# Kernel optimization log

Measured on AMD Instinct MI355X. Metric: run time of the kernel, lower is better.

The kernel has to match this reference:

```python
import jax, jax.numpy as jnp
import numpy as np

GRAPH_NUM = 2
HOP_K = 2
NODE_EMB_DIM = 16
INPUT_DIM = 2
HIDDEN = 64
B, N = 8, 400
IN_FEAT = INPUT_DIM + HIDDEN                      # 66, input to each MetaDGCN
I_DIM = (GRAPH_NUM * HOP_K + 1) * IN_FEAT         # 330


def setup_inputs() -> dict:
    key = jax.random.key(0)
    ks = jax.random.split(key, 8)
    x = jax.random.normal(ks[0], (B, N, INPUT_DIM), dtype=jnp.float32)
    state = jax.random.normal(ks[1], (B, N, HIDDEN), dtype=jnp.float32)
    graphs = jax.random.uniform(ks[2], (GRAPH_NUM, B, N, N), dtype=jnp.float32)
    # row-normalize like asym_adj so message passing is stable
    graphs = graphs / graphs.sum(-1, keepdims=True)
    node_emb = jax.random.normal(ks[3], (B, N, NODE_EMB_DIM), dtype=jnp.float32)
    s = 1.0 / np.sqrt(I_DIM)
    Wg = jax.random.normal(ks[4], (NODE_EMB_DIM, I_DIM, 2 * HIDDEN), dtype=jnp.float32) * s
    bg = jax.random.normal(ks[5], (NODE_EMB_DIM, 2 * HIDDEN), dtype=jnp.float32) * 0.1
    Wc = jax.random.normal(ks[6], (NODE_EMB_DIM, I_DIM, HIDDEN), dtype=jnp.float32) * s
    bc = jax.random.normal(ks[7], (NODE_EMB_DIM, HIDDEN), dtype=jnp.float32) * 0.1
    return {"x": x, "state": state, "graphs": graphs, "node_emb": node_emb,
            "Wg": Wg, "bg": bg, "Wc": Wc, "bc": bc}


def meta_dgcn(x, graphs, node_emb, weights_pool, bias_pool):
    # multi-hop propagation over each dynamic graph (GCN: 'bnm,bmd->bnd')
    out = [x]
    for i in range(GRAPH_NUM):
        x1 = x
        for _ in range(HOP_K):
            x1 = jnp.einsum('bnm,bmd->bnd', graphs[i], x1)
            out.append(x1)
    h = jnp.concatenate(out, axis=-1)                          # [B,N,I_DIM]
    # meta-generated per-node weights and bias
    weights = jnp.einsum('bnd,dio->bnio', node_emb, weights_pool)  # [B,N,I,O]
    bias = jnp.einsum('bnd,do->bno', node_emb, bias_pool)
    return jnp.einsum('bni,bnio->bno', h, weights) + bias


def reference(x, state, graphs, node_emb, Wg, bg, Wc, bc):
    # GRU-style meta-graph recurrent cell (MetaDGCRU)
    xs = jnp.concatenate([x, state], axis=-1)                  # [B,N,IN_FEAT]
    zr = jax.nn.sigmoid(meta_dgcn(xs, graphs, node_emb, Wg, bg))
    z, r = jnp.split(zr, 2, axis=-1)
    xrs = jnp.concatenate([x, r * state], axis=-1)
    hc = jnp.tanh(meta_dgcn(xrs, graphs, node_emb, Wc, bc))
    h = z * state + (1.0 - z) * hc                             # [B,N,HIDDEN]
    return h
```

## Files before the change

kernel.cpp:

```cpp
#include <hip/hip_runtime.h>
#include <hip/hip_bf16.h>
#include <math.h>

#define Bb 8
#define Nn 400
#define GN 2
#define INF 66
#define IDIM 330
#define KP 352
#define HID 64
#define EMB 16
#define NKP 416
#define XTR 80
constexpr int M = Bb * Nn;

typedef __attribute__((ext_vector_type(8))) short short8;
typedef __attribute__((ext_vector_type(4))) float f32x4;

__device__ __forceinline__ ushort f2bf(float f) {
    union { float f; unsigned u; } v; v.f = f;
    unsigned u = v.u;
    unsigned r = (u + 0x7FFFu + ((u >> 16) & 1u)) >> 16;
    return (ushort)r;
}

#define GBLKS 10400
__global__ void k_prep(const float* __restrict__ G, const float* __restrict__ Wg,
                       const float* __restrict__ Wc, const float* __restrict__ x,
                       const float* __restrict__ state,
                       ushort* __restrict__ Gbf, ushort* __restrict__ WgT,
                       ushort* __restrict__ WcT, ushort* __restrict__ Hbf,
                       ushort* __restrict__ XTin) {
    __shared__ float Tw[32][65];
    __shared__ ushort Tc[64][XTR + 1];
    int bid = blockIdx.x;
    if (bid < GBLKS) {
        size_t idx = (size_t)bid * 256 + threadIdx.x;
        int k = (int)(idx % NKP);
        size_t row = idx / NKP;
        Gbf[idx] = (k < Nn) ? f2bf(G[row * Nn + k]) : (ushort)0;
        return;
    }
    bid -= GBLKS;
    if (bid < 352 + 176) {
        const float* W; ushort* WT; int O;
        if (bid < 352) { W = Wg; WT = WgT; O = 128; }
        else           { bid -= 352; W = Wc; WT = WcT; O = 64; }
        const int k0 = (bid % 11) * 32;
        const int c0 = (bid / 11) * 64;
        const int d = c0 / O, o0 = c0 % O;
        for (int e = threadIdx.x; e < 2048; e += 256) {
            int kk = e >> 6, oo = e & 63;
            int k = k0 + kk;
            Tw[kk][oo] = (k < IDIM) ? W[((size_t)d * IDIM + k) * O + o0 + oo] : 0.f;
        }
        __syncthreads();
        for (int e = threadIdx.x; e < 2048; e += 256) {
            int cc = e >> 5, kk = e & 31;
            WT[(size_t)(c0 + cc) * KP + k0 + kk] = f2bf(Tw[kk][cc]);
        }
        return;
    }
    bid -= 528;
    const int b = bid / 7;
    const int k0 = (bid % 7) * 64;
    for (int e = threadIdx.x; e < 64 * XTR; e += 256) {
        int kk = e / XTR, c = e % XTR;
        int k = k0 + kk;
        ushort bf = 0;
        if (k < Nn && c < INF) {
            float v = (c < 2) ? x[((size_t)b * Nn + k) * 2 + c]
                              : state[((size_t)b * Nn + k) * HID + c - 2];
            bf = f2bf(v);
            Hbf[((size_t)b * Nn + k) * KP + c] = bf;
        }
        Tc[kk][c] = bf;
    }
    for (int e = threadIdx.x; e < 64 * 22; e += 256) {
        int kk = e / 22, c = 330 + e % 22;
        int k = k0 + kk;
        if (k < Nn) Hbf[((size_t)b * Nn + k) * KP + c] = 0;
    }
    __syncthreads();
    for (int e = threadIdx.x; e < XTR * 64; e += 256) {
        int c = e / 64, kk = e % 64;
        int k = k0 + kk;
        if (k < NKP) XTin[((size_t)b * XTR + c) * NKP + k] = Tc[kk][c];
    }
}

__global__ __launch_bounds__(64) void k_hop(const ushort* __restrict__ Gbf,
                      const ushort* __restrict__ XT,
                      ushort* __restrict__ Hbf, ushort* __restrict__ XTnext,
                      int out_base, int xt_per_g) {
    const int b = blockIdx.y, g = blockIdx.z;
    const int row0 = blockIdx.x * 16;
    const int lane = threadIdx.x;
    const int lr = lane & 15, kq = lane >> 4;

    const ushort* Gb = Gbf + (size_t)(g * Bb + b) * Nn * NKP;
    const ushort* Xb = XT + (size_t)((xt_per_g ? g * Bb : 0) + b) * XTR * NKP;
    const ushort* Grow = Gb + (size_t)(row0 + lr) * NKP;

    f32x4 acc[5] = {};
#pragma unroll
    for (int ks = 0; ks < 13; ++ks) {
        short8 af = *(const short8*)(Grow + ks * 32 + kq * 8);
#pragma unroll
        for (int n = 0; n < 5; ++n) {
            short8 bv = *(const short8*)(Xb + (size_t)(n * 16 + lr) * NKP + ks * 32 + kq * 8);
            acc[n] = __builtin_amdgcn_mfma_f32_16x16x32_bf16(af, bv, acc[n], 0, 0, 0);
        }
    }

    const int rbase = row0 + kq * 4;
    ushort* Hout = Hbf + (size_t)b * Nn * KP + out_base + g * 132;
#pragma unroll
    for (int n = 0; n < 5; ++n) {
        int col = n * 16 + lr;
        if (col < INF) {
#pragma unroll
            for (int r = 0; r < 4; ++r)
                Hout[(size_t)(rbase + r) * KP + col] = f2bf(acc[n][r]);
        }
    }
    if (XTnext) {
        ushort* Xn = XTnext + (size_t)(g * Bb + b) * XTR * NKP;
#pragma unroll
        for (int n = 0; n < 5; ++n) {
            int col = n * 16 + lr;
            ushort4 w;
#pragma unroll
            for (int r = 0; r < 4; ++r)
                w[r] = (col < INF) ? f2bf(acc[n][r]) : (ushort)0;
            *(ushort4*)(Xn + (size_t)col * NKP + rbase) = w;
        }
    }
}

template <int O>
__global__ __launch_bounds__(256, 3) void k_meta_fused(const ushort* __restrict__ Hbf,
        const ushort* __restrict__ WT, const float* __restrict__ emb,
        float* __restrict__ P) {
    constexpr int NB = O / 32;
    constexpr int PB = O / 64;
    __shared__ ushort As[2][64][40];
    __shared__ ushort Bs[2][2][O][40];
    const int ds = blockIdx.x;
    const int bm = blockIdx.y * 64;
    const int t = threadIdx.x;
    const int wid = t >> 6, lane = t & 63;
    const int wm = wid >> 1, wn = wid & 1;
    const int lr = lane & 15, kq = lane >> 4;

    const int ar = t >> 2, akc = (t & 3) * 8;
    const ushort* srcA = Hbf + (size_t)(bm + ar) * KP + akc;
    const ushort* srcB[2][PB];
    int brow[PB], bkc[PB];
#pragma unroll
    for (int p = 0; p < PB; ++p) {
        int chunk = t + p * 256;
        brow[p] = chunk >> 2; bkc[p] = (chunk & 3) * 8;
#pragma unroll
        for (int j = 0; j < 2; ++j)
            srcB[j][p] = WT + ((size_t)(ds * 2 + j) * O + brow[p]) * KP + bkc[p];
    }

    short8 ra, rb[2][PB];
    ra = *(const short8*)srcA;
#pragma unroll
    for (int j = 0; j < 2; ++j)
#pragma unroll
        for (int p = 0; p < PB; ++p) rb[j][p] = *(const short8*)srcB[j][p];

    f32x4 seg[2][2][NB] = {};

    for (int ks = 0; ks < 11; ++ks) {
        const int buf = ks & 1;
        *(short8*)&As[buf][ar][akc] = ra;
#pragma unroll
        for (int j = 0; j < 2; ++j)
#pragma unroll
            for (int p = 0; p < PB; ++p) *(short8*)&Bs[buf][j][brow[p]][bkc[p]] = rb[j][p];
        if (ks < 10) {
            const int k0 = (ks + 1) * 32;
            ra = *(const short8*)(srcA + k0);
#pragma unroll
            for (int j = 0; j < 2; ++j)
#pragma unroll
                for (int p = 0; p < PB; ++p) rb[j][p] = *(const short8*)(srcB[j][p] + k0);
        }
        __syncthreads();
        short8 a[2], bf[2][NB];
#pragma unroll
        for (int m = 0; m < 2; ++m)
            a[m] = *(const short8*)&As[buf][wm * 32 + m * 16 + lr][kq * 8];
#pragma unroll
        for (int j = 0; j < 2; ++j)
#pragma unroll
            for (int n = 0; n < NB; ++n)
                bf[j][n] = *(const short8*)&Bs[buf][j][wn * (O / 2) + n * 16 + lr][kq * 8];
#pragma unroll
        for (int j = 0; j < 2; ++j)
#pragma unroll
            for (int m = 0; m < 2; ++m)
#pragma unroll
                for (int n = 0; n < NB; ++n)
                    seg[j][m][n] = __builtin_amdgcn_mfma_f32_16x16x32_bf16(a[m], bf[j][n], seg[j][m][n], 0, 0, 0);
    }

    float* Pd = P + (size_t)ds * M * O;
#pragma unroll
    for (int m = 0; m < 2; ++m) {
        const int rbase = bm + wm * 32 + m * 16 + kq * 4;
#pragma unroll
        for (int r = 0; r < 4; ++r) {
            const int row = rbase + r;
            float e0 = emb[(size_t)row * EMB + ds * 2];
            float e1 = emb[(size_t)row * EMB + ds * 2 + 1];
#pragma unroll
            for (int n = 0; n < NB; ++n) {
                const int col = wn * (O / 2) + n * 16 + lr;
                Pd[(size_t)row * O + col] = e0 * seg[0][m][n][r] + e1 * seg[1][m][n][r];
            }
        }
    }
}

__global__ void k_zr(const float* __restrict__ P, const float* __restrict__ emb,
                     const float* __restrict__ bg, const float* __restrict__ state,
                     float* __restrict__ zbuf, ushort* __restrict__ Hbf,
                     ushort* __restrict__ XTin) {
    __shared__ float es[2][EMB];
    const int t = threadIdx.x;
    if (t < 2 * EMB) es[t >> 4][t & 15] = emb[((size_t)blockIdx.x * 2 + (t >> 4)) * EMB + (t & 15)];
    __syncthreads();
    const int node = blockIdx.x * 2 + (t >> 7);
    const int o = t & 127;
    float v = 0.f;
#pragma unroll
    for (int s = 0; s < 8; ++s) v += P[((size_t)s * M + node) * 128 + o];
    const float* e_ = es[t >> 7];
#pragma unroll
    for (int d = 0; d < EMB; ++d) v += e_[d] * bg[d * 128 + o];
    float sg = 1.f / (1.f + expf(-v));
    if (o < 64) {
        zbuf[node * 64 + o] = sg;
    } else {
        int oo = o - 64;
        ushort bf = f2bf(sg * state[node * 64 + oo]);
        Hbf[(size_t)node * KP + 2 + oo] = bf;
        int b = node / Nn, kn = node % Nn;
        XTin[((size_t)b * XTR + 2 + oo) * NKP + kn] = bf;
    }
}

__global__ void k_final(const float* __restrict__ P, const float* __restrict__ emb,
                        const float* __restrict__ bc, const float* __restrict__ zbuf,
                        const float* __restrict__ state, float* __restrict__ out) {
    __shared__ float es[4][EMB];
    const int t = threadIdx.x;
    if (t < 4 * EMB) es[t >> 4][t & 15] = emb[((size_t)blockIdx.x * 4 + (t >> 4)) * EMB + (t & 15)];
    __syncthreads();
    const int node = blockIdx.x * 4 + (t >> 6);
    const int o = t & 63;
    float v = 0.f;
#pragma unroll
    for (int s = 0; s < 8; ++s) v += P[((size_t)s * M + node) * 64 + o];
    const float* e_ = es[t >> 6];
#pragma unroll
    for (int d = 0; d < EMB; ++d) v += e_[d] * bc[d * 64 + o];
    float hc = tanhf(v);
    float z = zbuf[node * 64 + o];
    out[node * 64 + o] = z * state[node * 64 + o] + (1.f - z) * hc;
}

extern "C" void kernel_launch(void* const* d_in, const int* in_sizes, int n_in,
                              void* d_out, int out_size, void* d_ws, size_t ws_size,
                              hipStream_t stream) {
    const float* x      = (const float*)d_in[0];
    const float* state  = (const float*)d_in[1];
    const float* graphs = (const float*)d_in[2];
    const float* emb    = (const float*)d_in[3];
    const float* Wg     = (const float*)d_in[4];
    const float* bg     = (const float*)d_in[5];
    const float* Wc     = (const float*)d_in[6];
    const float* bc     = (const float*)d_in[7];
    float* out = (float*)d_out;

    char* ws = (char*)d_ws;
    ushort* Hbf  = (ushort*)ws;  ws += (size_t)M * KP * 2;
    ushort* Gbf  = (ushort*)ws;  ws += (size_t)GN * Bb * Nn * NKP * 2;
    ushort* WgT  = (ushort*)ws;  ws += (size_t)2048 * KP * 2;
    ushort* WcT  = (ushort*)ws;  ws += (size_t)1024 * KP * 2;
    ushort* XTin = (ushort*)ws;  ws += (size_t)Bb * XTR * NKP * 2;
    ushort* XTmid= (ushort*)ws;  ws += (size_t)GN * Bb * XTR * NKP * 2;
    float*  PG   = (float*)ws;   ws += (size_t)8 * M * 128 * 4;
    float*  PC   = (float*)ws;   ws += (size_t)8 * M * 64 * 4;
    float*  zb   = (float*)ws;

    dim3 hopgrid(25, Bb, GN);

    k_prep<<<10984, 256, 0, stream>>>(graphs, Wg, Wc, x, state, Gbf, WgT, WcT, Hbf, XTin);

    k_hop<<<hopgrid, 64, 0, stream>>>(Gbf, XTin, Hbf, XTmid, 66, 0);
    k_hop<<<hopgrid, 64, 0, stream>>>(Gbf, XTmid, Hbf, nullptr, 132, 1);
    k_meta_fused<128><<<dim3(8, 50), 256, 0, stream>>>(Hbf, WgT, emb, PG);
    k_zr<<<1600, 256, 0, stream>>>(PG, emb, bg, state, zb, Hbf, XTin);

    k_hop<<<hopgrid, 64, 0, stream>>>(Gbf, XTin, Hbf, XTmid, 66, 0);
    k_hop<<<hopgrid, 64, 0, stream>>>(Gbf, XTmid, Hbf, nullptr, 132, 1);
    k_meta_fused<64><<<dim3(8, 50), 256, 0, stream>>>(Hbf, WcT, emb, PC);
    k_final<<<800, 256, 0, stream>>>(PC, emb, bc, zb, state, out);
}
```

Baseline: 75.45 us.

## Fuse meta-weight GEMM with embedding reduction and gate epilogues; widen hop tiles

Replaces the per-embedding-pair GEMM that wrote partial products to global memory, along with the separate k_zr and k_final reduction kernels, with one kernel per gate. Each block covers all 16 embedding dims for a 32x32 output tile and reduces across waves in shared memory before applying the bias and sigmoid/tanh epilogue. The hop kernel now computes 32 rows per block with clamped loads and guarded stores, and a second H buffer avoids a write hazard between the gate and candidate passes. This removes the large fp32 partial buffers and two launches, but the smaller tiles re-read the weights far more often and the MFMA kernel uses more registers.

Result: slower. 107.0 us (+41.8%).

```diff
diff --git a/kernel.cpp b/kernel.cpp
--- a/kernel.cpp
+++ b/kernel.cpp
@@ -30,7 +30,7 @@
                        const float* __restrict__ state,
                        ushort* __restrict__ Gbf, ushort* __restrict__ WgT,
                        ushort* __restrict__ WcT, ushort* __restrict__ Hbf,
-                       ushort* __restrict__ XTin) {
+                       ushort* __restrict__ Hbf2, ushort* __restrict__ XTin) {
     __shared__ float Tw[32][65];
     __shared__ ushort Tc[64][XTR + 1];
     int bid = blockIdx.x;
@@ -73,13 +73,17 @@
                               : state[((size_t)b * Nn + k) * HID + c - 2];
             bf = f2bf(v);
             Hbf[((size_t)b * Nn + k) * KP + c] = bf;
+            if (c < 2) Hbf2[((size_t)b * Nn + k) * KP + c] = bf;
         }
         Tc[kk][c] = bf;
     }
     for (int e = threadIdx.x; e < 64 * 22; e += 256) {
         int kk = e / 22, c = 330 + e % 22;
         int k = k0 + kk;
-        if (k < Nn) Hbf[((size_t)b * Nn + k) * KP + c] = 0;
+        if (k < Nn) {
+            Hbf[((size_t)b * Nn + k) * KP + c] = 0;
+            Hbf2[((size_t)b * Nn + k) * KP + c] = 0;
+        }
     }
     __syncthreads();
     for (int e = threadIdx.x; e < XTR * 64; e += 256) {
@@ -91,188 +95,177 @@
 
 __global__ __launch_bounds__(64) void k_hop(const ushort* __restrict__ Gbf,
                       const ushort* __restrict__ XT,
-                      ushort* __restrict__ Hbf, ushort* __restrict__ XTnext,
+                      ushort* __restrict__ Hb, ushort* __restrict__ XTnext,
                       int out_base, int xt_per_g) {
     const int b = blockIdx.y, g = blockIdx.z;
-    const int row0 = blockIdx.x * 16;
+    const int row0 = blockIdx.x * 32;
     const int lane = threadIdx.x;
     const int lr = lane & 15, kq = lane >> 4;
 
     const ushort* Gb = Gbf + (size_t)(g * Bb + b) * Nn * NKP;
     const ushort* Xb = XT + (size_t)((xt_per_g ? g * Bb : 0) + b) * XTR * NKP;
-    const ushort* Grow = Gb + (size_t)(row0 + lr) * NKP;
-
-    f32x4 acc[5] = {};
+    int ar0 = row0 + lr;        if (ar0 > Nn - 1) ar0 = Nn - 1;
+    int ar1 = row0 + 16 + lr;   if (ar1 > Nn - 1) ar1 = Nn - 1;
+    const ushort* Gr0 = Gb + (size_t)ar0 * NKP;
+    const ushort* Gr1 = Gb + (size_t)ar1 * NKP;
+
+    f32x4 acc[2][5] = {};
 #pragma unroll
     for (int ks = 0; ks < 13; ++ks) {
-        short8 af = *(const short8*)(Grow + ks * 32 + kq * 8);
+        short8 a0 = *(const short8*)(Gr0 + ks * 32 + kq * 8);
+        short8 a1 = *(const short8*)(Gr1 + ks * 32 + kq * 8);
 #pragma unroll
         for (int n = 0; n < 5; ++n) {
             short8 bv = *(const short8*)(Xb + (size_t)(n * 16 + lr) * NKP + ks * 32 + kq * 8);
-            acc[n] = __builtin_amdgcn_mfma_f32_16x16x32_bf16(af, bv, acc[n], 0, 0, 0);
-        }
-    }
-
-    const int rbase = row0 + kq * 4;
-    ushort* Hout = Hbf + (size_t)b * Nn * KP + out_base + g * 132;
-#pragma unroll
-    for (int n = 0; n < 5; ++n) {
-        int col = n * 16 + lr;
-        if (col < INF) {
-#pragma unroll
-            for (int r = 0; r < 4; ++r)
-                Hout[(size_t)(rbase + r) * KP + col] = f2bf(acc[n][r]);
+            acc[0][n] = __builtin_amdgcn_mfma_f32_16x16x32_bf16(a0, bv, acc[0][n], 0, 0, 0);
+            acc[1][n] = __builtin_amdgcn_mfma_f32_16x16x32_bf16(a1, bv, acc[1][n], 0, 0, 0);
+        }
+    }
+
+    ushort* Hout = Hb + (size_t)b * Nn * KP + out_base + g * 132;
+#pragma unroll
+    for (int tt = 0; tt < 2; ++tt) {
+        const int rbase = row0 + tt * 16 + kq * 4;
+#pragma unroll
+        for (int n = 0; n < 5; ++n) {
+            int col = n * 16 + lr;
+            if (col < INF) {
+#pragma unroll
+                for (int r = 0; r < 4; ++r) {
+                    int row = rbase + r;
+                    if (row < Nn) Hout[(size_t)row * KP + col] = f2bf(acc[tt][n][r]);
+                }
+            }
         }
     }
     if (XTnext) {
         ushort* Xn = XTnext + (size_t)(g * Bb + b) * XTR * NKP;
 #pragma unroll
-        for (int n = 0; n < 5; ++n) {
-            int col = n * 16 + lr;
-            ushort4 w;
-#pragma unroll
-            for (int r = 0; r < 4; ++r)
-                w[r] = (col < INF) ? f2bf(acc[n][r]) : (ushort)0;
-            *(ushort4*)(Xn + (size_t)col * NKP + rbase) = w;
-        }
-    }
-}
-
-template <int O>
-__global__ __launch_bounds__(256, 3) void k_meta_fused(const ushort* __restrict__ Hbf,
-        const ushort* __restrict__ WT, const float* __restrict__ emb,
-        float* __restrict__ P) {
-    constexpr int NB = O / 32;
-    constexpr int PB = O / 64;
-    __shared__ ushort As[2][64][40];
-    __shared__ ushort Bs[2][2][O][40];
-    const int ds = blockIdx.x;
-    const int bm = blockIdx.y * 64;
+        for (int tt = 0; tt < 2; ++tt) {
+            const int rbase = row0 + tt * 16 + kq * 4;
+#pragma unroll
+            for (int n = 0; n < 5; ++n) {
+                int col = n * 16 + lr;
+                ushort4 w;
+#pragma unroll
+                for (int r = 0; r < 4; ++r)
+                    w[r] = (col < INF) ? f2bf(acc[tt][n][r]) : (ushort)0;
+                *(ushort4*)(Xn + (size_t)col * NKP + rbase) = w;
+            }
+        }
+    }
+}
+
+template <int O, int MODE>
+__global__ __launch_bounds__(256) void k_meta_all(
+    const ushort* __restrict__ Hsrc, const ushort* __restrict__ WT,
+    const float* __restrict__ emb, const float* __restrict__ bias,
+    const float* __restrict__ state, float* __restrict__ zb,
+    float* __restrict__ out, ushort* __restrict__ Hdst, ushort* __restrict__ XTin) {
+    __shared__ ushort As[32][40];
+    __shared__ ushort Bs[16][32][40];
+    __shared__ float es[32][EMB];
+    const int bo = blockIdx.x * 32, bm = blockIdx.y * 32;
     const int t = threadIdx.x;
-    const int wid = t >> 6, lane = t & 63;
-    const int wm = wid >> 1, wn = wid & 1;
-    const int lr = lane & 15, kq = lane >> 4;
+    const int wq = t >> 6, lane = t & 63, lr = lane & 15, kq = lane >> 4;
+
+    {
+        int idx = t * 2;
+        float2 ev = *(const float2*)(emb + (size_t)bm * EMB + idx);
+        es[idx >> 4][idx & 15] = ev.x;
+        es[idx >> 4][(idx & 15) + 1] = ev.y;
+    }
 
     const int ar = t >> 2, akc = (t & 3) * 8;
-    const ushort* srcA = Hbf + (size_t)(bm + ar) * KP + akc;
-    const ushort* srcB[2][PB];
-    int brow[PB], bkc[PB];
-#pragma unroll
-    for (int p = 0; p < PB; ++p) {
-        int chunk = t + p * 256;
-        brow[p] = chunk >> 2; bkc[p] = (chunk & 3) * 8;
-#pragma unroll
-        for (int j = 0; j < 2; ++j)
-            srcB[j][p] = WT + ((size_t)(ds * 2 + j) * O + brow[p]) * KP + bkc[p];
-    }
-
-    short8 ra, rb[2][PB];
-    ra = *(const short8*)srcA;
-#pragma unroll
-    for (int j = 0; j < 2; ++j)
-#pragma unroll
-        for (int p = 0; p < PB; ++p) rb[j][p] = *(const short8*)srcB[j][p];
-
-    f32x4 seg[2][2][NB] = {};
-
+    const ushort* srcA = Hsrc + (size_t)(bm + ar) * KP + akc;
+    int bd[8], bcol[8], bkc[8];
+    const ushort* srcB[8];
+#pragma unroll
+    for (int p = 0; p < 8; ++p) {
+        int c = t + p * 256;
+        bd[p] = c >> 7; bcol[p] = (c >> 2) & 31; bkc[p] = (c & 3) * 8;
+        srcB[p] = WT + ((size_t)(bd[p] * O + bo + bcol[p])) * KP + bkc[p];
+    }
+
+    short8 rA, rB[8];
+    if (t < 128) rA = *(const short8*)srcA;
+#pragma unroll
+    for (int p = 0; p < 8; ++p) rB[p] = *(const short8*)srcB[p];
+
+    f32x4 seg[4][2][2] = {};
     for (int ks = 0; ks < 11; ++ks) {
-        const int buf = ks & 1;
-        *(short8*)&As[buf][ar][akc] = ra;
-#pragma unroll
-        for (int j = 0; j < 2; ++j)
-#pragma unroll
-            for (int p = 0; p < PB; ++p) *(short8*)&Bs[buf][j][brow[p]][bkc[p]] = rb[j][p];
+        if (t < 128) *(short8*)&As[ar][akc] = rA;
+#pragma unroll
+        for (int p = 0; p < 8; ++p) *(short8*)&Bs[bd[p]][bcol[p]][bkc[p]] = rB[p];
+        __syncthreads();
         if (ks < 10) {
             const int k0 = (ks + 1) * 32;
-            ra = *(const short8*)(srcA + k0);
-#pragma unroll
-            for (int j = 0; j < 2; ++j)
-#pragma unroll
-                for (int p = 0; p < PB; ++p) rb[j][p] = *(const short8*)(srcB[j][p] + k0);
-        }
+            if (t < 128) rA = *(const short8*)(srcA + k0);
+#pragma unroll
+            for (int p = 0; p < 8; ++p) rB[p] = *(const short8*)(srcB[p] + k0);
+        }
+        short8 a[2], bf[4][2];
+#pragma unroll
+        for (int m = 0; m < 2; ++m) a[m] = *(const short8*)&As[m * 16 + lr][kq * 8];
+#pragma unroll
+        for (int j = 0; j < 4; ++j)
+#pragma unroll
+            for (int n = 0; n < 2; ++n)
+                bf[j][n] = *(const short8*)&Bs[wq * 4 + j][n * 16 + lr][kq * 8];
+#pragma unroll
+        for (int j = 0; j < 4; ++j)
+#pragma unroll
+            for (int m = 0; m < 2; ++m)
+#pragma unroll
+                for (int n = 0; n < 2; ++n)
+                    seg[j][m][n] = __builtin_amdgcn_mfma_f32_16x16x32_bf16(a[m], bf[j][n], seg[j][m][n], 0, 0, 0);
         __syncthreads();
-        short8 a[2], bf[2][NB];
-#pragma unroll
-        for (int m = 0; m < 2; ++m)
-            a[m] = *(const short8*)&As[buf][wm * 32 + m * 16 + lr][kq * 8];
-#pragma unroll
-        for (int j = 0; j < 2; ++j)
-#pragma unroll
-            for (int n = 0; n < NB; ++n)
-                bf[j][n] = *(const short8*)&Bs[buf][j][wn * (O / 2) + n * 16 + lr][kq * 8];
-#pragma unroll
-        for (int j = 0; j < 2; ++j)
-#pragma unroll
-            for (int m = 0; m < 2; ++m)
-#pragma unroll
-                for (int n = 0; n < NB; ++n)
-                    seg[j][m][n] = __builtin_amdgcn_mfma_f32_16x16x32_bf16(a[m], bf[j][n], seg[j][m][n], 0, 0, 0);
-    }
-
-    float* Pd = P + (size_t)ds * M * O;
+    }
+
+    float* Red = (float*)&Bs[0][0][0];
 #pragma unroll
     for (int m = 0; m < 2; ++m) {
-        const int rbase = bm + wm * 32 + m * 16 + kq * 4;
 #pragma unroll
         for (int r = 0; r < 4; ++r) {
-            const int row = rbase + r;
-            float e0 = emb[(size_t)row * EMB + ds * 2];
-            float e1 = emb[(size_t)row * EMB + ds * 2 + 1];
-#pragma unroll
-            for (int n = 0; n < NB; ++n) {
-                const int col = wn * (O / 2) + n * 16 + lr;
-                Pd[(size_t)row * O + col] = e0 * seg[0][m][n][r] + e1 * seg[1][m][n][r];
+            const int row = m * 16 + kq * 4 + r;
+            const float e0 = es[row][wq * 4 + 0], e1 = es[row][wq * 4 + 1];
+            const float e2 = es[row][wq * 4 + 2], e3 = es[row][wq * 4 + 3];
+#pragma unroll
+            for (int n = 0; n < 2; ++n) {
+                float v = e0 * seg[0][m][n][r] + e1 * seg[1][m][n][r]
+                        + e2 * seg[2][m][n][r] + e3 * seg[3][m][n][r];
+                Red[(wq * 32 + row) * 33 + n * 16 + lr] = v;
             }
         }
     }
-}
-
-__global__ void k_zr(const float* __restrict__ P, const float* __restrict__ emb,
-                     const float* __restrict__ bg, const float* __restrict__ state,
-                     float* __restrict__ zbuf, ushort* __restrict__ Hbf,
-                     ushort* __restrict__ XTin) {
-    __shared__ float es[2][EMB];
-    const int t = threadIdx.x;
-    if (t < 2 * EMB) es[t >> 4][t & 15] = emb[((size_t)blockIdx.x * 2 + (t >> 4)) * EMB + (t & 15)];
     __syncthreads();
-    const int node = blockIdx.x * 2 + (t >> 7);
-    const int o = t & 127;
-    float v = 0.f;
-#pragma unroll
-    for (int s = 0; s < 8; ++s) v += P[((size_t)s * M + node) * 128 + o];
-    const float* e_ = es[t >> 7];
-#pragma unroll
-    for (int d = 0; d < EMB; ++d) v += e_[d] * bg[d * 128 + o];
-    float sg = 1.f / (1.f + expf(-v));
-    if (o < 64) {
-        zbuf[node * 64 + o] = sg;
-    } else {
-        int oo = o - 64;
-        ushort bf = f2bf(sg * state[node * 64 + oo]);
-        Hbf[(size_t)node * KP + 2 + oo] = bf;
-        int b = node / Nn, kn = node % Nn;
-        XTin[((size_t)b * XTR + 2 + oo) * NKP + kn] = bf;
-    }
-}
-
-__global__ void k_final(const float* __restrict__ P, const float* __restrict__ emb,
-                        const float* __restrict__ bc, const float* __restrict__ zbuf,
-                        const float* __restrict__ state, float* __restrict__ out) {
-    __shared__ float es[4][EMB];
-    const int t = threadIdx.x;
-    if (t < 4 * EMB) es[t >> 4][t & 15] = emb[((size_t)blockIdx.x * 4 + (t >> 4)) * EMB + (t & 15)];
-    __syncthreads();
-    const int node = blockIdx.x * 4 + (t >> 6);
-    const int o = t & 63;
-    float v = 0.f;
-#pragma unroll
-    for (int s = 0; s < 8; ++s) v += P[((size_t)s * M + node) * 64 + o];
-    const float* e_ = es[t >> 6];
-#pragma unroll
-    for (int d = 0; d < EMB; ++d) v += e_[d] * bc[d * 64 + o];
-    float hc = tanhf(v);
-    float z = zbuf[node * 64 + o];
-    out[node * 64 + o] = z * state[node * 64 + o] + (1.f - z) * hc;
+
+#pragma unroll
+    for (int e4 = 0; e4 < 4; ++e4) {
+        const int idx = e4 * 256 + t;
+        const int row = idx >> 5, col = idx & 31;
+        float v = Red[row * 33 + col] + Red[(32 + row) * 33 + col]
+                + Red[(64 + row) * 33 + col] + Red[(96 + row) * 33 + col];
+#pragma unroll
+        for (int d = 0; d < EMB; ++d) v += es[row][d] * bias[d * O + bo + col];
+        const int node = bm + row, o = bo + col;
+        if (MODE == 0) {
+            float sg = 1.f / (1.f + expf(-v));
+            if (o < 64) {
+                zb[node * 64 + o] = sg;
+            } else {
+                int oo = o - 64;
+                ushort bfv = f2bf(sg * state[node * 64 + oo]);
+                Hdst[(size_t)node * KP + 2 + oo] = bfv;
+                int b = node / Nn, kn = node % Nn;
+                XTin[((size_t)b * XTR + 2 + oo) * NKP + kn] = bfv;
+            }
+        } else {
+            float hc = tanhf(v);
+            float z = zb[node * 64 + o];
+            out[node * 64 + o] = z * state[node * 64 + o] + (1.f - z) * hc;
+        }
+    }
 }
 
 extern "C" void kernel_launch(void* const* d_in, const int* in_sizes, int n_in,
@@ -290,26 +283,25 @@
 
     char* ws = (char*)d_ws;
     ushort* Hbf  = (ushort*)ws;  ws += (size_t)M * KP * 2;
+    ushort* Hbf2 = (ushort*)ws;  ws += (size_t)M * KP * 2;
     ushort* Gbf  = (ushort*)ws;  ws += (size_t)GN * Bb * Nn * NKP * 2;
     ushort* WgT  = (ushort*)ws;  ws += (size_t)2048 * KP * 2;
     ushort* WcT  = (ushort*)ws;  ws += (size_t)1024 * KP * 2;
     ushort* XTin = (ushort*)ws;  ws += (size_t)Bb * XTR * NKP * 2;
     ushort* XTmid= (ushort*)ws;  ws += (size_t)GN * Bb * XTR * NKP * 2;
-    float*  PG   = (float*)ws;   ws += (size_t)8 * M * 128 * 4;
-    float*  PC   = (float*)ws;   ws += (size_t)8 * M * 64 * 4;
     float*  zb   = (float*)ws;
 
-    dim3 hopgrid(25, Bb, GN);
-
-    k_prep<<<10984, 256, 0, stream>>>(graphs, Wg, Wc, x, state, Gbf, WgT, WcT, Hbf, XTin);
+    dim3 hopgrid(13, Bb, GN);
+
+    k_prep<<<10984, 256, 0, stream>>>(graphs, Wg, Wc, x, state, Gbf, WgT, WcT, Hbf, Hbf2, XTin);
 
     k_hop<<<hopgrid, 64, 0, stream>>>(Gbf, XTin, Hbf, XTmid, 66, 0);
     k_hop<<<hopgrid, 64, 0, stream>>>(Gbf, XTmid, Hbf, nullptr, 132, 1);
-    k_meta_fused<128><<<dim3(8, 50), 256, 0, stream>>>(Hbf, WgT, emb, PG);
-    k_zr<<<1600, 256, 0, stream>>>(PG, emb, bg, state, zb, Hbf, XTin);
-
-    k_hop<<<hopgrid, 64, 0, stream>>>(Gbf, XTin, Hbf, XTmid, 66, 0);
-    k_hop<<<hopgrid, 64, 0, stream>>>(Gbf, XTmid, Hbf, nullptr, 132, 1);
-    k_meta_fused<64><<<dim3(8, 50), 256, 0, stream>>>(Hbf, WcT, emb, PC);
-    k_final<<<800, 256, 0, stream>>>(PC, emb, bc, zb, state, out);
-}
+    k_meta_all<128, 0><<<dim3(4, 100), 256, 0, stream>>>(Hbf, WgT, emb, bg, state, zb,
+                                                         nullptr, Hbf2, XTin);
+
+    k_hop<<<hopgrid, 64, 0, stream>>>(Gbf, XTin, Hbf2, XTmid, 66, 0);
+    k_hop<<<hopgrid, 64, 0, stream>>>(Gbf, XTmid, Hbf2, nullptr, 132, 1);
+    k_meta_all<64, 1><<<dim3(2, 100), 256, 0, stream>>>(Hbf2, WcT, emb, bc, state, zb,
+                                                        out, nullptr, nullptr);
+}
```

## Split hop K-loop across four waves with LDS reduction; vectorize graph bf16 conversion

Applied to the files above, without the earlier changes.

The hop kernel now runs four waves per block. Each wave takes a strided subset of the 13 K-steps, and the partial accumulators are reduced through shared memory before wave 0 writes the outputs. This raises parallelism for the latency-bound 400-wide propagation GEMMs, which had only 400 single-wave blocks. It adds an LDS round trip and a barrier. Separately, the graph fp32-to-bf16 conversion in prep now handles four elements per thread with float4 loads and ushort4 stores, cutting the block count and the per-element index arithmetic.

Result: slower. 77.16 us (+2.3%).

```diff
diff --git a/kernel.cpp b/kernel.cpp
--- a/kernel.cpp
+++ b/kernel.cpp
@@ -24,7 +24,7 @@
     return (ushort)r;
 }
 
-#define GBLKS 10400
+#define GBLKS4 2600
 __global__ void k_prep(const float* __restrict__ G, const float* __restrict__ Wg,
                        const float* __restrict__ Wc, const float* __restrict__ x,
                        const float* __restrict__ state,
@@ -34,14 +34,21 @@
     __shared__ float Tw[32][65];
     __shared__ ushort Tc[64][XTR + 1];
     int bid = blockIdx.x;
-    if (bid < GBLKS) {
-        size_t idx = (size_t)bid * 256 + threadIdx.x;
-        int k = (int)(idx % NKP);
-        size_t row = idx / NKP;
-        Gbf[idx] = (k < Nn) ? f2bf(G[row * Nn + k]) : (ushort)0;
+    if (bid < GBLKS4) {
+        size_t tid4 = ((size_t)bid * 256 + threadIdx.x) * 4;
+        int k = (int)(tid4 % NKP);
+        size_t row = tid4 / NKP;
+        ushort4 o;
+        if (k < Nn) {
+            float4 gv = *(const float4*)(G + row * Nn + k);
+            o.x = f2bf(gv.x); o.y = f2bf(gv.y); o.z = f2bf(gv.z); o.w = f2bf(gv.w);
+        } else {
+            o.x = o.y = o.z = o.w = 0;
+        }
+        *(ushort4*)(Gbf + tid4) = o;
         return;
     }
-    bid -= GBLKS;
+    bid -= GBLKS4;
     if (bid < 352 + 176) {
         const float* W; ushort* WT; int O;
         if (bid < 352) { W = Wg; WT = WgT; O = 128; }
@@ -89,14 +96,15 @@
     }
 }
 
-__global__ __launch_bounds__(64) void k_hop(const ushort* __restrict__ Gbf,
+__global__ __launch_bounds__(256) void k_hop(const ushort* __restrict__ Gbf,
                       const ushort* __restrict__ XT,
-                      ushort* __restrict__ Hbf, ushort* __restrict__ XTnext,
+                      ushort* __restrict__ Hb, ushort* __restrict__ XTnext,
                       int out_base, int xt_per_g) {
     const int b = blockIdx.y, g = blockIdx.z;
     const int row0 = blockIdx.x * 16;
-    const int lane = threadIdx.x;
+    const int wid = threadIdx.x >> 6, lane = threadIdx.x & 63;
     const int lr = lane & 15, kq = lane >> 4;
+    __shared__ float Red[3][5][256];
 
     const ushort* Gb = Gbf + (size_t)(g * Bb + b) * Nn * NKP;
     const ushort* Xb = XT + (size_t)((xt_per_g ? g * Bb : 0) + b) * XTR * NKP;
@@ -104,36 +112,56 @@
 
     f32x4 acc[5] = {};
 #pragma unroll
-    for (int ks = 0; ks < 13; ++ks) {
-        short8 af = *(const short8*)(Grow + ks * 32 + kq * 8);
-#pragma unroll
-        for (int n = 0; n < 5; ++n) {
-            short8 bv = *(const short8*)(Xb + (size_t)(n * 16 + lr) * NKP + ks * 32 + kq * 8);
-            acc[n] = __builtin_amdgcn_mfma_f32_16x16x32_bf16(af, bv, acc[n], 0, 0, 0);
-        }
-    }
-
-    const int rbase = row0 + kq * 4;
-    ushort* Hout = Hbf + (size_t)b * Nn * KP + out_base + g * 132;
-#pragma unroll
-    for (int n = 0; n < 5; ++n) {
-        int col = n * 16 + lr;
-        if (col < INF) {
+    for (int i = 0; i < 4; ++i) {
+        const int ks = i * 4 + wid;
+        if (ks < 13) {
+            short8 af = *(const short8*)(Grow + ks * 32 + kq * 8);
+#pragma unroll
+            for (int n = 0; n < 5; ++n) {
+                short8 bv = *(const short8*)(Xb + (size_t)(n * 16 + lr) * NKP + ks * 32 + kq * 8);
+                acc[n] = __builtin_amdgcn_mfma_f32_16x16x32_bf16(af, bv, acc[n], 0, 0, 0);
+            }
+        }
+    }
+
+    if (wid) {
+#pragma unroll
+        for (int n = 0; n < 5; ++n)
 #pragma unroll
             for (int r = 0; r < 4; ++r)
-                Hout[(size_t)(rbase + r) * KP + col] = f2bf(acc[n][r]);
-        }
-    }
-    if (XTnext) {
-        ushort* Xn = XTnext + (size_t)(g * Bb + b) * XTR * NKP;
+                Red[wid - 1][n][(kq * 4 + r) * 16 + lr] = acc[n][r];
+    }
+    __syncthreads();
+    if (wid == 0) {
+#pragma unroll
+        for (int n = 0; n < 5; ++n)
+#pragma unroll
+            for (int r = 0; r < 4; ++r) {
+                const int idx = (kq * 4 + r) * 16 + lr;
+                acc[n][r] += Red[0][n][idx] + Red[1][n][idx] + Red[2][n][idx];
+            }
+        const int rbase = row0 + kq * 4;
+        ushort* Hout = Hb + (size_t)b * Nn * KP + out_base + g * 132;
 #pragma unroll
         for (int n = 0; n < 5; ++n) {
             int col = n * 16 + lr;
-            ushort4 w;
-#pragma unroll
-            for (int r = 0; r < 4; ++r)
-                w[r] = (col < INF) ? f2bf(acc[n][r]) : (ushort)0;
-            *(ushort4*)(Xn + (size_t)col * NKP + rbase) = w;
+            if (col < INF) {
+#pragma unroll
+                for (int r = 0; r < 4; ++r)
+                    Hout[(size_t)(rbase + r) * KP + col] = f2bf(acc[n][r]);
+            }
+        }
+        if (XTnext) {
+            ushort* Xn = XTnext + (size_t)(g * Bb + b) * XTR * NKP;
+#pragma unroll
+            for (int n = 0; n < 5; ++n) {
+                int col = n * 16 + lr;
+                ushort4 w;
+#pragma unroll
+                for (int r = 0; r < 4; ++r)
+                    w[r] = (col < INF) ? f2bf(acc[n][r]) : (ushort)0;
+                *(ushort4*)(Xn + (size_t)col * NKP + rbase) = w;
+            }
         }
     }
 }
@@ -301,15 +329,15 @@
 
     dim3 hopgrid(25, Bb, GN);
 
-    k_prep<<<10984, 256, 0, stream>>>(graphs, Wg, Wc, x, state, Gbf, WgT, WcT, Hbf, XTin);
-
-    k_hop<<<hopgrid, 64, 0, stream>>>(Gbf, XTin, Hbf, XTmid, 66, 0);
-    k_hop<<<hopgrid, 64, 0, stream>>>(Gbf, XTmid, Hbf, nullptr, 132, 1);
+    k_prep<<<3184, 256, 0, stream>>>(graphs, Wg, Wc, x, state, Gbf, WgT, WcT, Hbf, XTin);
+
+    k_hop<<<hopgrid, 256, 0, stream>>>(Gbf, XTin, Hbf, XTmid, 66, 0);
+    k_hop<<<hopgrid, 256, 0, stream>>>(Gbf, XTmid, Hbf, nullptr, 132, 1);
     k_meta_fused<128><<<dim3(8, 50), 256, 0, stream>>>(Hbf, WgT, emb, PG);
     k_zr<<<1600, 256, 0, stream>>>(PG, emb, bg, state, zb, Hbf, XTin);
 
-    k_hop<<<hopgrid, 64, 0, stream>>>(Gbf, XTin, Hbf, XTmid, 66, 0);
-    k_hop<<<hopgrid, 64, 0, stream>>>(Gbf, XTmid, Hbf, nullptr, 132, 1);
+    k_hop<<<hopgrid, 256, 0, stream>>>(Gbf, XTin, Hbf, XTmid, 66, 0);
+    k_hop<<<hopgrid, 256, 0, stream>>>(Gbf, XTmid, Hbf, nullptr, 132, 1);
     k_meta_fused<64><<<dim3(8, 50), 256, 0, stream>>>(Hbf, WcT, emb, PC);
     k_final<<<800, 256, 0, stream>>>(PC, emb, bc, zb, state, out);
 }
```

## Vectorize graph bf16 conversion and drop LDS staging in meta GEMM

Applied to the files above, without the earlier changes.

The graph fp32-to-bf16 conversion now processes four elements per thread with float4 loads and ushort4 stores, which cuts the prep grid size. The meta-weight GEMM no longer stages tiles through double-buffered shared memory with barriers. Each wave instead loads its MFMA fragments directly from global memory (L2/L1), removing LDS traffic and __syncthreads but relying on cache hits for the operands that waves share. The occupancy hint in launch_bounds is also removed.

After: 92.75 us. +22.9%, slower.

```diff
diff --git a/kernel.cpp b/kernel.cpp
--- a/kernel.cpp
+++ b/kernel.cpp
@@ -24,7 +24,7 @@
     return (ushort)r;
 }
 
-#define GBLKS 10400
+#define GBLKS4 2600
 __global__ void k_prep(const float* __restrict__ G, const float* __restrict__ Wg,
                        const float* __restrict__ Wc, const float* __restrict__ x,
                        const float* __restrict__ state,
@@ -34,14 +34,21 @@
     __shared__ float Tw[32][65];
     __shared__ ushort Tc[64][XTR + 1];
     int bid = blockIdx.x;
-    if (bid < GBLKS) {
-        size_t idx = (size_t)bid * 256 + threadIdx.x;
-        int k = (int)(idx % NKP);
-        size_t row = idx / NKP;
-        Gbf[idx] = (k < Nn) ? f2bf(G[row * Nn + k]) : (ushort)0;
+    if (bid < GBLKS4) {
+        size_t tid4 = ((size_t)bid * 256 + threadIdx.x) * 4;
+        int k = (int)(tid4 % NKP);
+        size_t row = tid4 / NKP;
+        ushort4 o;
+        if (k < Nn) {
+            float4 gv = *(const float4*)(G + row * Nn + k);
+            o.x = f2bf(gv.x); o.y = f2bf(gv.y); o.z = f2bf(gv.z); o.w = f2bf(gv.w);
+        } else {
+            o.x = o.y = o.z = o.w = 0;
+        }
+        *(ushort4*)(Gbf + tid4) = o;
         return;
     }
-    bid -= GBLKS;
+    bid -= GBLKS4;
     if (bid < 352 + 176) {
         const float* W; ushort* WT; int O;
         if (bid < 352) { W = Wg; WT = WgT; O = 128; }
@@ -91,7 +98,7 @@
 
 __global__ __launch_bounds__(64) void k_hop(const ushort* __restrict__ Gbf,
                       const ushort* __restrict__ XT,
-                      ushort* __restrict__ Hbf, ushort* __restrict__ XTnext,
+                      ushort* __restrict__ Hb, ushort* __restrict__ XTnext,
                       int out_base, int xt_per_g) {
     const int b = blockIdx.y, g = blockIdx.z;
     const int row0 = blockIdx.x * 16;
@@ -114,7 +121,7 @@
     }
 
     const int rbase = row0 + kq * 4;
-    ushort* Hout = Hbf + (size_t)b * Nn * KP + out_base + g * 132;
+    ushort* Hout = Hb + (size_t)b * Nn * KP + out_base + g * 132;
 #pragma unroll
     for (int n = 0; n < 5; ++n) {
         int col = n * 16 + lr;
@@ -139,13 +146,10 @@
 }
 
 template <int O>
-__global__ __launch_bounds__(256, 3) void k_meta_fused(const ushort* __restrict__ Hbf,
+__global__ __launch_bounds__(256) void k_meta_ng(const ushort* __restrict__ Hbf,
         const ushort* __restrict__ WT, const float* __restrict__ emb,
         float* __restrict__ P) {
     constexpr int NB = O / 32;
-    constexpr int PB = O / 64;
-    __shared__ ushort As[2][64][40];
-    __shared__ ushort Bs[2][2][O][40];
     const int ds = blockIdx.x;
     const int bm = blockIdx.y * 64;
     const int t = threadIdx.x;
@@ -153,60 +157,32 @@
     const int wm = wid >> 1, wn = wid & 1;
     const int lr = lane & 15, kq = lane >> 4;
 
-    const int ar = t >> 2, akc = (t & 3) * 8;
-    const ushort* srcA = Hbf + (size_t)(bm + ar) * KP + akc;
-    const ushort* srcB[2][PB];
-    int brow[PB], bkc[PB];
-#pragma unroll
-    for (int p = 0; p < PB; ++p) {
-        int chunk = t + p * 256;
-        brow[p] = chunk >> 2; bkc[p] = (chunk & 3) * 8;
+    const ushort* Arow[2];
+#pragma unroll
+    for (int m = 0; m < 2; ++m)
+        Arow[m] = Hbf + (size_t)(bm + wm * 32 + m * 16 + lr) * KP + kq * 8;
+    const ushort* Brow[2][NB];
+#pragma unroll
+    for (int j = 0; j < 2; ++j)
+#pragma unroll
+        for (int n = 0; n < NB; ++n)
+            Brow[j][n] = WT + (size_t)((ds * 2 + j) * O + wn * (O / 2) + n * 16 + lr) * KP + kq * 8;
+
+    f32x4 seg[2][2][NB] = {};
+#pragma unroll
+    for (int ks = 0; ks < 11; ++ks) {
+        short8 a[2];
+#pragma unroll
+        for (int m = 0; m < 2; ++m) a[m] = *(const short8*)(Arow[m] + ks * 32);
 #pragma unroll
         for (int j = 0; j < 2; ++j)
-            srcB[j][p] = WT + ((size_t)(ds * 2 + j) * O + brow[p]) * KP + bkc[p];
-    }
-
-    short8 ra, rb[2][PB];
-    ra = *(const short8*)srcA;
-#pragma unroll
-    for (int j = 0; j < 2; ++j)
-#pragma unroll
-        for (int p = 0; p < PB; ++p) rb[j][p] = *(const short8*)srcB[j][p];
-
-    f32x4 seg[2][2][NB] = {};
-
-    for (int ks = 0; ks < 11; ++ks) {
-        const int buf = ks & 1;
-        *(short8*)&As[buf][ar][akc] = ra;
-#pragma unroll
-        for (int j = 0; j < 2; ++j)
-#pragma unroll
-            for (int p = 0; p < PB; ++p) *(short8*)&Bs[buf][j][brow[p]][bkc[p]] = rb[j][p];
-        if (ks < 10) {
-            const int k0 = (ks + 1) * 32;
-            ra = *(const short8*)(srcA + k0);
-#pragma unroll
-            for (int j = 0; j < 2; ++j)
-#pragma unroll
-                for (int p = 0; p < PB; ++p) rb[j][p] = *(const short8*)(srcB[j][p] + k0);
-        }
-        __syncthreads();
-        short8 a[2], bf[2][NB];
-#pragma unroll
-        for (int m = 0; m < 2; ++m)
-            a[m] = *(const short8*)&As[buf][wm * 32 + m * 16 + lr][kq * 8];
-#pragma unroll
-        for (int j = 0; j < 2; ++j)
-#pragma unroll
-            for (int n = 0; n < NB; ++n)
-                bf[j][n] = *(const short8*)&Bs[buf][j][wn * (O / 2) + n * 16 + lr][kq * 8];
-#pragma unroll
-        for (int j = 0; j < 2; ++j)
-#pragma unroll
-            for (int m = 0; m < 2; ++m)
-#pragma unroll
-                for (int n = 0; n < NB; ++n)
-                    seg[j][m][n] = __builtin_amdgcn_mfma_f32_16x16x32_bf16(a[m], bf[j][n], seg[j][m][n], 0, 0, 0);
+#pragma unroll
+            for (int n = 0; n < NB; ++n) {
+                short8 bv = *(const short8*)(Brow[j][n] + ks * 32);
+#pragma unroll
+                for (int m = 0; m < 2; ++m)
+                    seg[j][m][n] = __builtin_amdgcn_mfma_f32_16x16x32_bf16(a[m], bv, seg[j][m][n], 0, 0, 0);
+            }
     }
 
     float* Pd = P + (size_t)ds * M * O;
@@ -301,15 +277,15 @@
 
     dim3 hopgrid(25, Bb, GN);
 
-    k_prep<<<10984, 256, 0, stream>>>(graphs, Wg, Wc, x, state, Gbf, WgT, WcT, Hbf, XTin);
+    k_prep<<<3184, 256, 0, stream>>>(graphs, Wg, Wc, x, state, Gbf, WgT, WcT, Hbf, XTin);
 
     k_hop<<<hopgrid, 64, 0, stream>>>(Gbf, XTin, Hbf, XTmid, 66, 0);
     k_hop<<<hopgrid, 64, 0, stream>>>(Gbf, XTmid, Hbf, nullptr, 132, 1);
-    k_meta_fused<128><<<dim3(8, 50), 256, 0, stream>>>(Hbf, WgT, emb, PG);
+    k_meta_ng<128><<<dim3(8, 50), 256, 0, stream>>>(Hbf, WgT, emb, PG);
     k_zr<<<1600, 256, 0, stream>>>(PG, emb, bg, state, zb, Hbf, XTin);
 
     k_hop<<<hopgrid, 64, 0, stream>>>(Gbf, XTin, Hbf, XTmid, 66, 0);
     k_hop<<<hopgrid, 64, 0, stream>>>(Gbf, XTmid, Hbf, nullptr, 132, 1);
-    k_meta_fused<64><<<dim3(8, 50), 256, 0, stream>>>(Hbf, WcT, emb, PC);
+    k_meta_ng<64><<<dim3(8, 50), 256, 0, stream>>>(Hbf, WcT, emb, PC);
     k_final<<<800, 256, 0, stream>>>(PC, emb, bc, zb, state, out);
 }
```
